# Performance work log

Hardware: AMD Instinct MI355X
Metric: run time of the kernel (lower is better)

The kernel has to match this reference:

```python
import jax, jax.numpy as jnp
import numpy as np

V = 5023      # CoMA mesh vertices
K = 8         # avg neighbors per vertex
E = V * K     # edges
B = 64        # batch
C_IN = 3      # xyz
C_HID = 64    # conv width (layer_info)
M = 9         # kernel_size: number of weight matrices
LATENT = 128


def fsc_conv(x, src, dst, aw, u, c, W, b):
    """Feature-steered graph conv (translation invariant: v = -u).
    x: [B,V,C]; edge e: (i=src[e], j=dst[e]) with adjacency weight aw[e].
    y_i = b + sum_j a_ij * sum_m softmax_m(u_m.(x_i-x_j)+c_m) * (x_j @ W_m)
    """
    Bx, Vx, C = x.shape
    D = W.shape[2]
    xi = x[:, src]                                  # [B,E,C]
    xj = x[:, dst]                                  # [B,E,C]
    logits = jnp.einsum('bec,cm->bem', xi - xj, u) + c   # [B,E,M]
    att = jax.nn.softmax(logits, axis=-1) * aw[None, :, None]
    y = jnp.zeros((Bx, Vx, D), x.dtype)
    for m in range(W.shape[0]):                     # small fixed loop over M
        agg = jnp.zeros((Bx, Vx, C), x.dtype).at[:, src].add(att[:, :, m:m + 1] * xj)
        y = y + agg @ W[m]
    return y + b


def setup_inputs() -> dict:
    key = jax.random.key(0)
    ks = jax.random.split(key, 16)
    x = jax.random.normal(ks[0], (B, V, C_IN), jnp.float32)
    # mesh-like adjacency: each vertex i has K random neighbors, weight 1/K
    src = jnp.repeat(jnp.arange(V, dtype=jnp.int32), K)
    dst = jax.random.randint(ks[1], (E,), 0, V, dtype=jnp.int32)
    aw = jnp.full((E,), 1.0 / K, jnp.float32)
    g = lambda k, shp, fan: jax.random.normal(k, shp, jnp.float32) * np.float32(np.sqrt(2.0 / fan))
    # encoder conv params
    u_e = g(ks[2], (C_IN, M), C_IN + M)
    c_e = jnp.zeros((M,), jnp.float32)
    W_e = g(ks[3], (M, C_IN, C_HID), C_IN + C_HID)
    b_e = jnp.zeros((C_HID,), jnp.float32)
    # encoder latent dense: [V*C_HID, LATENT]
    W_enc = g(ks[4], (V * C_HID, LATENT), V * C_HID)
    b_enc = jnp.zeros((LATENT,), jnp.float32)
    # decoder latent dense: [LATENT, C_HID*V]
    W_dec = g(ks[5], (LATENT, C_HID * V), LATENT)
    b_dec = jnp.zeros((C_HID * V,), jnp.float32)
    # decoder conv params
    u_d = g(ks[6], (C_HID, M), C_HID + M)
    c_d = jnp.zeros((M,), jnp.float32)
    W_d = g(ks[7], (M, C_HID, C_IN), C_HID + C_IN)
    b_d = jnp.zeros((C_IN,), jnp.float32)
    return {'x': x, 'aw': aw, 'u_e': u_e, 'c_e': c_e, 'W_e': W_e, 'b_e': b_e,
            'W_enc': W_enc, 'b_enc': b_enc, 'W_dec': W_dec, 'b_dec': b_dec,
            'u_d': u_d, 'c_d': c_d, 'W_d': W_d, 'b_d': b_d,
            'src': src, 'dst': dst}


def reference(x, aw, u_e, c_e, W_e, b_e, W_enc, b_enc, W_dec, b_dec,
              u_d, c_d, W_d, b_d, src, dst):
    # Encoder: feature-steered conv -> relu -> flatten -> dense to latent
    h = jax.nn.relu(fsc_conv(x, src, dst, aw, u_e, c_e, W_e, b_e))   # [B,V,C_HID]
    z = h.reshape(h.shape[0], -1) @ W_enc + b_enc                    # [B,LATENT]
    # Decoder: dense -> reshape [B,V,C_HID] -> feature-steered conv -> relu
    d = (z @ W_dec + b_dec).reshape(z.shape[0], V, -1)               # [B,V,C_HID]
    out = jax.nn.relu(fsc_conv(d, src, dst, aw, u_d, c_d, W_d, b_d)) # [B,V,3]
    return out
```

## Files before the change

kernel.cpp:

```cpp
#include <hip/hip_runtime.h>

#define VN 5023
#define KN 8
#define BN 64
#define CIN 3
#define CH 64
#define MN 9
#define LAT 128
#define KTOT (VN*CH)
#define NBV (BN*VN)
#define KC 256
#define NCHUNK 1256
#define RED_G 8
#define RED_J 157
#define NXCD 8

__global__ __launch_bounds__(256, 4) void k_conv1(
    const float* __restrict__ x, const float* __restrict__ aw,
    const int* __restrict__ dst,
    const float* __restrict__ u_e, const float* __restrict__ c_e,
    const float* __restrict__ W_e, const float* __restrict__ b_e,
    float* __restrict__ h)
{
  int t = blockIdx.x*256 + threadIdx.x;
  if (t >= NBV) return;
  int b = t / VN, v = t - b*VN;
  const float* xb = x + (size_t)b*VN*CIN;
  int e0 = v*KN;
  int4 j01 = *(const int4*)(dst + e0);
  int4 j23 = *(const int4*)(dst + e0 + 4);
  int jj[8] = {j01.x,j01.y,j01.z,j01.w, j23.x,j23.y,j23.z,j23.w};
  float4 a01 = *(const float4*)(aw + e0);
  float4 a23 = *(const float4*)(aw + e0 + 4);
  float awv[8] = {a01.x,a01.y,a01.z,a01.w, a23.x,a23.y,a23.z,a23.w};
  float xj0[8], xj1[8], xj2[8];
#pragma unroll
  for (int k=0;k<KN;k++){
    const float* xr = xb + (size_t)jj[k]*3;
    xj0[k]=xr[0]; xj1[k]=xr[1]; xj2[k]=xr[2];
  }
  __builtin_amdgcn_sched_barrier(0);
  float xi0 = xb[v*3+0], xi1 = xb[v*3+1], xi2 = xb[v*3+2];
  float Ti[MN];
#pragma unroll
  for (int m=0;m<MN;m++)
    Ti[m] = xi0*u_e[m] + xi1*u_e[MN+m] + xi2*u_e[2*MN+m] + c_e[m];
  float agg[27];
#pragma unroll
  for (int i=0;i<27;i++) agg[i]=0.f;
#pragma unroll
  for (int k=0;k<KN;k++){
    float lg[MN];
#pragma unroll
    for (int m=0;m<MN;m++)
      lg[m] = Ti[m] - (xj0[k]*u_e[m]+xj1[k]*u_e[MN+m]+xj2[k]*u_e[2*MN+m]);
    float mx = lg[0];
#pragma unroll
    for (int m=1;m<MN;m++) mx = fmaxf(mx, lg[m]);
    float ex[MN], s=0.f;
#pragma unroll
    for (int m=0;m<MN;m++){ ex[m] = __expf(lg[m]-mx); s += ex[m]; }
    float r = awv[k] / s;
#pragma unroll
    for (int m=0;m<MN;m++){
      float a = ex[m]*r;
      agg[m*3+0] += a*xj0[k]; agg[m*3+1] += a*xj1[k]; agg[m*3+2] += a*xj2[k];
    }
  }
  float* hr = h + (size_t)t*CH;
  for (int cc=0; cc<4; cc++){
    float y[16];
#pragma unroll
    for (int c=0;c<16;c++) y[c] = b_e[cc*16+c];
#pragma unroll
    for (int mc=0; mc<27; mc++){
      float a = agg[mc];
#pragma unroll
      for (int c=0;c<16;c++) y[c] += a * W_e[mc*CH + cc*16 + c];
    }
#pragma unroll
    for (int c=0;c<16;c+=4){
      float4 o = make_float4(fmaxf(y[c],0.f),fmaxf(y[c+1],0.f),
                             fmaxf(y[c+2],0.f),fmaxf(y[c+3],0.f));
      *(float4*)(hr + cc*16 + c) = o;
    }
  }
}

__global__ __launch_bounds__(256, 4) void k_enc(
    const float* __restrict__ h, const float* __restrict__ We,
    float* __restrict__ partial)
{
  __shared__ float wlds[2][32*128];
  __shared__ float hlds[2][32][68];
  int t = threadIdx.x;
  int blk = blockIdx.x;
  int lq = t & 15;
  int bq = t >> 4;
  float acc[8][4];
#pragma unroll
  for (int i=0;i<8;i++)
#pragma unroll
    for (int j=0;j<4;j++) acc[i][j]=0.f;
  int kbase0 = blk*KC;
  int ldb = t & 63;
  int seg = t >> 6;
  int nt0 = (blk == NCHUNK-1) ? 6 : 8;

  float4 wreg0, wreg1, wreg2, wreg3, hreg0, hreg1;
  {
    const float* wsrc = We + (size_t)kbase0*LAT;
    wreg0 = *(const float4*)(wsrc + 0*1024 + t*4);
    wreg1 = *(const float4*)(wsrc + 1*1024 + t*4);
    wreg2 = *(const float4*)(wsrc + 2*1024 + t*4);
    wreg3 = *(const float4*)(wsrc + 3*1024 + t*4);
    const float* hsrc = h + (size_t)ldb*KTOT + kbase0 + seg*8;
    hreg0 = *(const float4*)(hsrc);
    hreg1 = *(const float4*)(hsrc + 4);
    *(float4*)(&wlds[0][0*1024 + t*4]) = wreg0;
    *(float4*)(&wlds[0][1*1024 + t*4]) = wreg1;
    *(float4*)(&wlds[0][2*1024 + t*4]) = wreg2;
    *(float4*)(&wlds[0][3*1024 + t*4]) = wreg3;
    hlds[0][seg*8+0][ldb]=hreg0.x; hlds[0][seg*8+1][ldb]=hreg0.y;
    hlds[0][seg*8+2][ldb]=hreg0.z; hlds[0][seg*8+3][ldb]=hreg0.w;
    hlds[0][seg*8+4][ldb]=hreg1.x; hlds[0][seg*8+5][ldb]=hreg1.y;
    hlds[0][seg*8+6][ldb]=hreg1.z; hlds[0][seg*8+7][ldb]=hreg1.w;
  }
  __syncthreads();

  int cur = 0;
  for (int t0=0; t0<nt0; t0++){
    bool pf = (t0+1 < nt0);
    if (pf){
      int kbase = kbase0 + (t0+1)*32;
      const float* wsrc = We + (size_t)kbase*LAT;
      wreg0 = *(const float4*)(wsrc + 0*1024 + t*4);
      wreg1 = *(const float4*)(wsrc + 1*1024 + t*4);
      wreg2 = *(const float4*)(wsrc + 2*1024 + t*4);
      wreg3 = *(const float4*)(wsrc + 3*1024 + t*4);
      const float* hsrc = h + (size_t)ldb*KTOT + kbase + seg*8;
      hreg0 = *(const float4*)(hsrc);
      hreg1 = *(const float4*)(hsrc + 4);
    }
    __builtin_amdgcn_sched_barrier(0);
#pragma unroll 4
    for (int kk=0; kk<32; kk++){
      float4 w0 = *(const float4*)(&wlds[cur][kk*128 + lq*4]);
      float4 w1 = *(const float4*)(&wlds[cur][kk*128 + 64 + lq*4]);
      float4 z  = *(const float4*)(&hlds[cur][kk][bq*4]);
      float wv[8] = {w0.x,w0.y,w0.z,w0.w,w1.x,w1.y,w1.z,w1.w};
      float zv[4] = {z.x,z.y,z.z,z.w};
#pragma unroll
      for (int li=0;li<8;li++)
#pragma unroll
        for (int bi=0;bi<4;bi++) acc[li][bi] += wv[li]*zv[bi];
    }
    if (pf){
      int nb = cur^1;
      *(float4*)(&wlds[nb][0*1024 + t*4]) = wreg0;
      *(float4*)(&wlds[nb][1*1024 + t*4]) = wreg1;
      *(float4*)(&wlds[nb][2*1024 + t*4]) = wreg2;
      *(float4*)(&wlds[nb][3*1024 + t*4]) = wreg3;
      hlds[nb][seg*8+0][ldb]=hreg0.x; hlds[nb][seg*8+1][ldb]=hreg0.y;
      hlds[nb][seg*8+2][ldb]=hreg0.z; hlds[nb][seg*8+3][ldb]=hreg0.w;
      hlds[nb][seg*8+4][ldb]=hreg1.x; hlds[nb][seg*8+5][ldb]=hreg1.y;
      hlds[nb][seg*8+6][ldb]=hreg1.z; hlds[nb][seg*8+7][ldb]=hreg1.w;
    }
    __syncthreads();
    cur ^= 1;
  }
  float* pp = partial + (size_t)blk*(BN*LAT);
#pragma unroll
  for (int bi=0;bi<4;bi++){
    int b = bq*4+bi;
    float4 o0 = make_float4(acc[0][bi],acc[1][bi],acc[2][bi],acc[3][bi]);
    float4 o1 = make_float4(acc[4][bi],acc[5][bi],acc[6][bi],acc[7][bi]);
    *(float4*)(pp + b*LAT + lq*4)      = o0;
    *(float4*)(pp + b*LAT + 64 + lq*4) = o1;
  }
}

__global__ __launch_bounds__(256) void k_red1(
    const float* __restrict__ partial, float* __restrict__ partial2)
{
  int idx = blockIdx.x*256 + threadIdx.x;
  int g = blockIdx.y;
  float s = 0.f;
  for (int j=0;j<RED_J;j++)
    s += partial[(size_t)(g + RED_G*j)*(BN*LAT) + idx];
  partial2[(size_t)g*(BN*LAT) + idx] = s;
}

__global__ __launch_bounds__(256) void k_red2(
    const float* __restrict__ partial2, const float* __restrict__ b_enc,
    float* __restrict__ zT)
{
  int idx = blockIdx.x*256 + threadIdx.x;
  float s = 0.f;
#pragma unroll
  for (int g=0; g<RED_G; g++) s += partial2[(size_t)g*(BN*LAT) + idx];
  int b = idx >> 7, l = idx & 127;
  zT[l*BN + b] = s + b_enc[l];
}

__global__ __launch_bounds__(256, 4) void k_dec(
    const float* __restrict__ zT, const float* __restrict__ Wd,
    const float* __restrict__ b_dec, float* __restrict__ d)
{
  int t = threadIdx.x;
  int lane = t & 63;
  int wv = __builtin_amdgcn_readfirstlane(t >> 6);
  int vc = blockIdx.x*256 + lane*4;
  int vs = vc < (KTOT-4) ? vc : (KTOT-4);
  const float* wp = Wd + vs;
  const float* zrow = zT + wv*16;
  float acc[4][16];
#pragma unroll
  for (int i=0;i<4;i++)
#pragma unroll
    for (int j=0;j<16;j++) acc[i][j]=0.f;

  float4 wA[4], wB[4];
#pragma unroll
  for (int u=0;u<4;u++) wA[u] = *(const float4*)(wp + (size_t)u*KTOT);

  for (int l0=0; l0<LAT; l0+=8){
#pragma unroll
    for (int u=0;u<4;u++) wB[u] = *(const float4*)(wp + (size_t)(l0+4+u)*KTOT);
    __builtin_amdgcn_sched_barrier(0);
#pragma unroll
    for (int u=0;u<4;u++){
      int l = l0+u;
      float zv[16];
#pragma unroll
      for (int j=0;j<16;j++) zv[j] = zrow[l*BN + j];
      float wvv[4] = {wA[u].x,wA[u].y,wA[u].z,wA[u].w};
#pragma unroll
      for (int i=0;i<4;i++)
#pragma unroll
        for (int j=0;j<16;j++) acc[i][j] += wvv[i]*zv[j];
    }
    if (l0+8 < LAT){
#pragma unroll
      for (int u=0;u<4;u++) wA[u] = *(const float4*)(wp + (size_t)(l0+8+u)*KTOT);
    }
    __builtin_amdgcn_sched_barrier(0);
#pragma unroll
    for (int u=0;u<4;u++){
      int l = l0+4+u;
      float zv[16];
#pragma unroll
      for (int j=0;j<16;j++) zv[j] = zrow[l*BN + j];
      float wvv[4] = {wB[u].x,wB[u].y,wB[u].z,wB[u].w};
#pragma unroll
      for (int i=0;i<4;i++)
#pragma unroll
        for (int j=0;j<16;j++) acc[i][j] += wvv[i]*zv[j];
    }
  }
  if (vc < KTOT){
    float4 bd = *(const float4*)(b_dec + vc);
#pragma unroll
    for (int j=0;j<16;j++){
      int b = wv*16 + j;
      float4 o = make_float4(acc[0][j]+bd.x, acc[1][j]+bd.y,
                             acc[2][j]+bd.z, acc[3][j]+bd.w);
      *(float4*)(d + (size_t)b*KTOT + vc) = o;
    }
  }
}

__global__ __launch_bounds__(256, 4) void k_tg(
    const float* __restrict__ d, const float* __restrict__ u_d,
    const float* __restrict__ W_d, float* __restrict__ TG)
{
  int t = blockIdx.x*256 + threadIdx.x;
  if (t >= NBV) return;
  const float* drow = d + (size_t)t*CH;
  float T[MN], G[27];
#pragma unroll
  for (int m=0;m<MN;m++) T[m]=0.f;
#pragma unroll
  for (int i=0;i<27;i++) G[i]=0.f;
  for (int c0=0;c0<CH;c0+=4){
    float4 dv = *(const float4*)(drow+c0);
    float dvv[4] = {dv.x,dv.y,dv.z,dv.w};
#pragma unroll
    for (int j=0;j<4;j++){
      int c = c0+j;
      float xv = dvv[j];
#pragma unroll
      for (int m=0;m<MN;m++) T[m] += xv*u_d[c*MN+m];
#pragma unroll
      for (int m=0;m<MN;m++){
        G[m*3+0] += xv*W_d[(m*CH+c)*3+0];
        G[m*3+1] += xv*W_d[(m*CH+c)*3+1];
        G[m*3+2] += xv*W_d[(m*CH+c)*3+2];
      }
    }
  }
  float* tg = TG + (size_t)t*36;
  float rr[36] = {T[0],T[1],T[2],T[3],T[4],T[5],T[6],T[7],T[8],
                  G[0],G[1],G[2],G[3],G[4],G[5],G[6],G[7],G[8],
                  G[9],G[10],G[11],G[12],G[13],G[14],G[15],G[16],G[17],
                  G[18],G[19],G[20],G[21],G[22],G[23],G[24],G[25],G[26]};
#pragma unroll
  for (int i=0;i<36;i+=4)
    *(float4*)(tg+i) = make_float4(rr[i],rr[i+1],rr[i+2],rr[i+3]);
}

__global__ __launch_bounds__(256, 4) void k_att(
    const float* __restrict__ TG, const float* __restrict__ aw,
    const int* __restrict__ dst, const float* __restrict__ c_d,
    const float* __restrict__ b_d, float* __restrict__ out)
{
  int wg = blockIdx.x;
  int wgid = (wg & 7)*157 + (wg >> 3);
  int t = wgid*256 + threadIdx.x;
  if (t >= NBV) return;
  int b = t / VN, v = t - b*VN;
  const float* TGb = TG + (size_t)b*VN*36;
  int e0 = v*KN;
  int4 j01 = *(const int4*)(dst + e0);
  int4 j23 = *(const int4*)(dst + e0 + 4);
  int jj[8] = {j01.x,j01.y,j01.z,j01.w, j23.x,j23.y,j23.z,j23.w};
  float4 a01 = *(const float4*)(aw + e0);
  float4 a23 = *(const float4*)(aw + e0 + 4);
  float awv[8] = {a01.x,a01.y,a01.z,a01.w, a23.x,a23.y,a23.z,a23.w};
  float Ti[MN];
#pragma unroll
  for (int m=0;m<MN;m++) Ti[m] = TGb[(size_t)v*36+m] + c_d[m];
  float y0=0.f, y1=0.f, y2=0.f;
  float4 q[9];
  {
    const float* Rp = TGb + (size_t)jj[0]*36;
#pragma unroll
    for (int i=0;i<9;i++) q[i] = *(const float4*)(Rp + i*4);
  }
#pragma unroll
  for (int k=0;k<KN;k++){
    float4 p[9];
    if (k+1 < KN){
      const float* Rp = TGb + (size_t)jj[k+1]*36;
#pragma unroll
      for (int i=0;i<9;i++) p[i] = *(const float4*)(Rp + i*4);
    }
    float rr[36] = {q[0].x,q[0].y,q[0].z,q[0].w, q[1].x,q[1].y,q[1].z,q[1].w,
                    q[2].x,q[2].y,q[2].z,q[2].w, q[3].x,q[3].y,q[3].z,q[3].w,
                    q[4].x,q[4].y,q[4].z,q[4].w, q[5].x,q[5].y,q[5].z,q[5].w,
                    q[6].x,q[6].y,q[6].z,q[6].w, q[7].x,q[7].y,q[7].z,q[7].w,
                    q[8].x,q[8].y,q[8].z,q[8].w};
    float lg[MN];
#pragma unroll
    for (int m=0;m<MN;m++) lg[m] = Ti[m] - rr[m];
    float mx = lg[0];
#pragma unroll
    for (int m=1;m<MN;m++) mx = fmaxf(mx, lg[m]);
    float ex[MN], s=0.f;
#pragma unroll
    for (int m=0;m<MN;m++){ ex[m] = __expf(lg[m]-mx); s += ex[m]; }
    float sc = awv[k] / s;
#pragma unroll
    for (int m=0;m<MN;m++){
      float a = ex[m]*sc;
      y0 += a*rr[9+m*3+0]; y1 += a*rr[9+m*3+1]; y2 += a*rr[9+m*3+2];
    }
    if (k+1 < KN){
#pragma unroll
      for (int i=0;i<9;i++) q[i] = p[i];
    }
  }
  float* o = out + (size_t)t*3;
  o[0]=fmaxf(y0+b_d[0],0.f); o[1]=fmaxf(y1+b_d[1],0.f); o[2]=fmaxf(y2+b_d[2],0.f);
}

extern "C" void kernel_launch(void* const* d_in, const int* in_sizes, int n_in,
                              void* d_out, int out_size, void* d_ws, size_t ws_size,
                              hipStream_t stream) {
  const float* x     = (const float*)d_in[0];
  const float* aw    = (const float*)d_in[1];
  const float* u_e   = (const float*)d_in[2];
  const float* c_e   = (const float*)d_in[3];
  const float* W_e   = (const float*)d_in[4];
  const float* b_e   = (const float*)d_in[5];
  const float* W_enc = (const float*)d_in[6];
  const float* b_enc = (const float*)d_in[7];
  const float* W_dec = (const float*)d_in[8];
  const float* b_dec = (const float*)d_in[9];
  const float* u_d   = (const float*)d_in[10];
  const float* c_d   = (const float*)d_in[11];
  const float* W_d   = (const float*)d_in[12];
  const float* b_d   = (const float*)d_in[13];
  const int*   dst   = (const int*)d_in[15];
  float* out = (float*)d_out;

  char* ws = (char*)d_ws;
  float* hbuf = (float*)ws;
  size_t off1 = (size_t)NBV*CH*sizeof(float);
  float* partial = (float*)(ws + off1);
  float* TGbuf   = (float*)(ws + off1);
  size_t offz = off1 + (size_t)NCHUNK*(BN*LAT)*sizeof(float) + 4096;
  float* zT       = (float*)(ws + offz);
  float* partial2 = (float*)(ws + offz + (size_t)(BN*LAT)*sizeof(float));

  int grid_bv = (NBV + 255)/256;

  k_conv1<<<grid_bv,256,0,stream>>>(x, aw, dst, u_e, c_e, W_e, b_e, hbuf);
  k_enc<<<NCHUNK,256,0,stream>>>(hbuf, W_enc, partial);
  dim3 gr1(32, RED_G);
  k_red1<<<gr1,256,0,stream>>>(partial, partial2);
  k_red2<<<32,256,0,stream>>>(partial2, b_enc, zT);
  int grid_dec = (KTOT + 255)/256;
  k_dec<<<grid_dec,256,0,stream>>>(zT, W_dec, b_dec, hbuf);
  k_tg<<<grid_bv,256,0,stream>>>(hbuf, u_d, W_d, TGbuf);
  k_att<<<grid_bv,256,0,stream>>>(TGbuf, aw, dst, c_d, b_d, out);
}
```

Baseline: 329.5 us.

## Fuse decoder dense layer with per-vertex TG projection through shared memory

```diff
diff --git a/kernel.cpp b/kernel.cpp
--- a/kernel.cpp
+++ b/kernel.cpp
@@ -203,14 +203,17 @@
   zT[l*BN + b] = s + b_enc[l];
 }
 
-__global__ __launch_bounds__(256, 4) void k_dec(
+__global__ __launch_bounds__(256, 4) void k_dectg(
     const float* __restrict__ zT, const float* __restrict__ Wd,
-    const float* __restrict__ b_dec, float* __restrict__ d)
-{
+    const float* __restrict__ b_dec, const float* __restrict__ u_d,
+    const float* __restrict__ W_d, float* __restrict__ TG)
+{
+  __shared__ float dt[4][256][8];
   int t = threadIdx.x;
   int lane = t & 63;
   int wv = __builtin_amdgcn_readfirstlane(t >> 6);
-  int vc = blockIdx.x*256 + lane*4;
+  int blk = blockIdx.x;
+  int vc = blk*256 + lane*4;
   int vs = vc < (KTOT-4) ? vc : (KTOT-4);
   const float* wp = Wd + vs;
   const float* zrow = zT + wv*16;
@@ -258,55 +261,52 @@
         for (int j=0;j<16;j++) acc[i][j] += wvv[i]*zv[j];
     }
   }
-  if (vc < KTOT){
-    float4 bd = *(const float4*)(b_dec + vc);
-#pragma unroll
-    for (int j=0;j<16;j++){
-      int b = wv*16 + j;
-      float4 o = make_float4(acc[0][j]+bd.x, acc[1][j]+bd.y,
-                             acc[2][j]+bd.z, acc[3][j]+bd.w);
-      *(float4*)(d + (size_t)b*KTOT + vc) = o;
-    }
-  }
-}
-
-__global__ __launch_bounds__(256, 4) void k_tg(
-    const float* __restrict__ d, const float* __restrict__ u_d,
-    const float* __restrict__ W_d, float* __restrict__ TG)
-{
-  int t = blockIdx.x*256 + threadIdx.x;
-  if (t >= NBV) return;
-  const float* drow = d + (size_t)t*CH;
-  float T[MN], G[27];
-#pragma unroll
-  for (int m=0;m<MN;m++) T[m]=0.f;
-#pragma unroll
-  for (int i=0;i<27;i++) G[i]=0.f;
-  for (int c0=0;c0<CH;c0+=4){
-    float4 dv = *(const float4*)(drow+c0);
-    float dvv[4] = {dv.x,dv.y,dv.z,dv.w};
-#pragma unroll
-    for (int j=0;j<4;j++){
-      int c = c0+j;
-      float xv = dvv[j];
-#pragma unroll
-      for (int m=0;m<MN;m++) T[m] += xv*u_d[c*MN+m];
-#pragma unroll
-      for (int m=0;m<MN;m++){
-        G[m*3+0] += xv*W_d[(m*CH+c)*3+0];
-        G[m*3+1] += xv*W_d[(m*CH+c)*3+1];
-        G[m*3+2] += xv*W_d[(m*CH+c)*3+2];
+  float4 bd = *(const float4*)(b_dec + vs);
+  float bdv[4] = {bd.x, bd.y, bd.z, bd.w};
+
+#pragma unroll
+  for (int hh=0; hh<2; hh++){
+#pragma unroll
+    for (int i=0;i<4;i++){
+      *(float4*)(&dt[wv][lane*4+i][0]) =
+        make_float4(acc[i][hh*8+0]+bdv[i], acc[i][hh*8+1]+bdv[i],
+                    acc[i][hh*8+2]+bdv[i], acc[i][hh*8+3]+bdv[i]);
+      *(float4*)(&dt[wv][lane*4+i][4]) =
+        make_float4(acc[i][hh*8+4]+bdv[i], acc[i][hh*8+5]+bdv[i],
+                    acc[i][hh*8+6]+bdv[i], acc[i][hh*8+7]+bdv[i]);
+    }
+    __syncthreads();
+    if (lane < 32){
+      int vl = lane >> 3, bl = lane & 7;
+      int vg = blk*4 + vl;
+      if (vg < VN){
+        float Tg[36];
+#pragma unroll
+        for (int q=0;q<36;q++) Tg[q]=0.f;
+#pragma unroll 2
+        for (int c=0;c<CH;c++){
+          float dv = dt[wv][vl*64 + c][bl];
+          const float* ur = u_d + c*MN;
+#pragma unroll
+          for (int m=0;m<MN;m++) Tg[m] += dv*ur[m];
+#pragma unroll
+          for (int m=0;m<MN;m++){
+            const float* wr = W_d + (m*CH + c)*3;
+            Tg[9+m*3+0] += dv*wr[0];
+            Tg[9+m*3+1] += dv*wr[1];
+            Tg[9+m*3+2] += dv*wr[2];
+          }
+        }
+        int bg = wv*16 + hh*8 + bl;
+        float* tg = TG + (size_t)((size_t)bg*VN + vg)*36;
+#pragma unroll
+        for (int q=0;q<9;q++)
+          *(float4*)(tg + q*4) = make_float4(Tg[q*4+0],Tg[q*4+1],
+                                             Tg[q*4+2],Tg[q*4+3]);
       }
     }
-  }
-  float* tg = TG + (size_t)t*36;
-  float rr[36] = {T[0],T[1],T[2],T[3],T[4],T[5],T[6],T[7],T[8],
-                  G[0],G[1],G[2],G[3],G[4],G[5],G[6],G[7],G[8],
-                  G[9],G[10],G[11],G[12],G[13],G[14],G[15],G[16],G[17],
-                  G[18],G[19],G[20],G[21],G[22],G[23],G[24],G[25],G[26]};
-#pragma unroll
-  for (int i=0;i<36;i+=4)
-    *(float4*)(tg+i) = make_float4(rr[i],rr[i+1],rr[i+2],rr[i+3]);
+    __syncthreads();
+  }
 }
 
 __global__ __launch_bounds__(256, 4) void k_att(
@@ -396,12 +396,11 @@
 
   char* ws = (char*)d_ws;
   float* hbuf = (float*)ws;
+  float* zT   = (float*)ws;
+  float* partial2 = (float*)(ws + (64<<10));
   size_t off1 = (size_t)NBV*CH*sizeof(float);
   float* partial = (float*)(ws + off1);
   float* TGbuf   = (float*)(ws + off1);
-  size_t offz = off1 + (size_t)NCHUNK*(BN*LAT)*sizeof(float) + 4096;
-  float* zT       = (float*)(ws + offz);
-  float* partial2 = (float*)(ws + offz + (size_t)(BN*LAT)*sizeof(float));
 
   int grid_bv = (NBV + 255)/256;
 
@@ -411,7 +410,6 @@
   k_red1<<<gr1,256,0,stream>>>(partial, partial2);
   k_red2<<<32,256,0,stream>>>(partial2, b_enc, zT);
   int grid_dec = (KTOT + 255)/256;
-  k_dec<<<grid_dec,256,0,stream>>>(zT, W_dec, b_dec, hbuf);
-  k_tg<<<grid_bv,256,0,stream>>>(hbuf, u_d, W_d, TGbuf);
+  k_dectg<<<grid_dec,256,0,stream>>>(zT, W_dec, b_dec, u_d, W_d, TGbuf);
   k_att<<<grid_bv,256,0,stream>>>(TGbuf, aw, dst, c_d, b_d, out);
 }
```

New measurement: 312.7 us. 1.05x faster.
